# Kernel optimization log

Hardware: AMD Instinct MI355X
Metric: run time of the kernel (lower is better)

The kernel has to match this reference:

```python
import jax, jax.numpy as jnp
import numpy as np

NUM_EMBEDDINGS = 1024
EMBEDDING_DIM = 64
COMMITMENT_COST = 0.25


def setup_inputs() -> dict:
    key = jax.random.key(0)
    k1, k2 = jax.random.split(key)
    inputs = jax.random.normal(k1, (64, 2048, EMBEDDING_DIM), dtype=jnp.float32)
    # nn.Embedding weight init: uniform(-1/K, 1/K)
    lim = 1.0 / NUM_EMBEDDINGS
    weight = jax.random.uniform(k2, (NUM_EMBEDDINGS, EMBEDDING_DIM),
                                dtype=jnp.float32, minval=-lim, maxval=lim)
    return {"inputs": inputs, "weight": weight}


def reference(inputs, weight):
    # inputs: [B, T, D], weight: [K, D]
    flat = inputs.reshape(-1, EMBEDDING_DIM)              # [N, D]
    distances = (jnp.sum(flat * flat, axis=1, keepdims=True)
                 + jnp.sum(weight * weight, axis=1)
                 - 2.0 * flat @ weight.T)
    encoding_indices = jnp.argmin(distances, axis=1)[:, None]  # [N, 1]
    quantized = weight[encoding_indices[:, 0]].reshape(inputs.shape)
    # detached quantized vs inputs (commitment), quantized vs detached inputs (codebook)
    e_latent_loss = jnp.mean((jax.lax.stop_gradient(quantized) - inputs) ** 2)
    q_latent_loss = jnp.mean((quantized - jax.lax.stop_gradient(inputs)) ** 2)
    loss = q_latent_loss + COMMITMENT_COST * e_latent_loss
    # straight-through estimator
    quantized_st = inputs + jax.lax.stop_gradient(quantized - inputs)
    return (loss, quantized_st, encoding_indices)
```

## Files before the change

kernel.cpp:

```cpp
#include <hip/hip_runtime.h>

#define NROWS   131072
#define DIM     64
#define K       1024
#define QOFF    1
#define IDXOFF  8388609
#define NSCR    2048
#define NFIN    512

typedef float    f32x4 __attribute__((ext_vector_type(4)));
typedef _Float16 f16x8 __attribute__((ext_vector_type(8)));

__device__ __forceinline__ float np_norm64(const float* v) {
    #pragma clang fp contract(off)
    float r[8];
    #pragma unroll
    for (int k = 0; k < 8; ++k) r[k] = v[k] * v[k];
    #pragma unroll
    for (int i = 8; i < 64; i += 8)
        #pragma unroll
        for (int k = 0; k < 8; ++k) r[k] += v[i + k] * v[i + k];
    return ((r[0] + r[1]) + (r[2] + r[3])) + ((r[4] + r[5]) + (r[6] + r[7]));
}
__device__ __forceinline__ float exact_dot64(const float* xr, const float* __restrict__ e) {
    float a0 = 0.f, a1 = 0.f, a2 = 0.f, a3 = 0.f;
    #pragma unroll
    for (int i = 0; i < 64; i += 4) {
        a0 = fmaf(xr[i + 0], e[i + 0], a0);
        a1 = fmaf(xr[i + 1], e[i + 1], a1);
        a2 = fmaf(xr[i + 2], e[i + 2], a2);
        a3 = fmaf(xr[i + 3], e[i + 3], a3);
    }
    return (a0 + a1) + (a2 + a3);
}
__device__ __forceinline__ float exact_d(float cr, float sej, float dot) {
    #pragma clang fp contract(off)
    float t = cr + sej;
    return t - 2.0f * dot;
}

__global__ void vq_prep(const float* __restrict__ w, unsigned short* __restrict__ Gf,
                        float* __restrict__ wT, float* __restrict__ se,
                        float* __restrict__ se20) {
    int gid = blockIdx.x * 256 + threadIdx.x;
    int lane = gid & 63, c = (gid >> 6) & 1, ntile = gid >> 7;
    int code = ntile * 16 + (lane & 15);
    int k0 = c * 32 + (lane >> 4) * 8;
    const float* rowp = w + code * 64 + k0;
    f16x8 h8;
    #pragma unroll
    for (int j = 0; j < 8; ++j) h8[j] = (_Float16)(rowp[j] * 1024.0f);
    *(f16x8*)(Gf + gid * 8) = h8;
    #pragma unroll
    for (int t = 0; t < 8; ++t) {
        int flat = t * 8192 + gid;
        int i = flat >> 10, j = flat & 1023;
        wT[flat] = w[j * 64 + i];
    }
    if (gid < K) {
        #pragma clang fp contract(off)
        const float* e = w + gid * 64;
        float r[8];
        #pragma unroll
        for (int k2 = 0; k2 < 8; ++k2) r[k2] = e[k2] * e[k2];
        #pragma unroll
        for (int i = 8; i < 64; i += 8)
            #pragma unroll
            for (int k2 = 0; k2 < 8; ++k2) r[k2] += e[i + k2] * e[i + k2];
        float v = ((r[0] + r[1]) + (r[2] + r[3])) + ((r[4] + r[5]) + (r[6] + r[7]));
        se[gid] = v;
        se20[gid] = v * 1048576.0f;
    }
}

__global__ __launch_bounds__(256, 8) void vq_screen(
    const float* __restrict__ x, const float* __restrict__ w,
    const unsigned short* __restrict__ Gf, const float* __restrict__ se20,
    float* __restrict__ out, float* __restrict__ partial, int* __restrict__ gcnt,
    int* __restrict__ pairRows, int* __restrict__ pairJJ, int* __restrict__ fullRows) {
    __shared__ float sSe[1024];
    __shared__ float sPart[4];
    __shared__ int sCnt[2], sBase[2];
    __shared__ int sPairRow[64], sPairJJ[64], sFullRow[64];
    const int tid  = threadIdx.x;
    const int wave = tid >> 6, lane = tid & 63;
    const int quad = lane >> 4, m16 = lane & 15;
    const int wrow0 = blockIdx.x * 64 + wave * 16;

    if (tid < 2) sCnt[tid] = 0;
    #pragma unroll
    for (int t = 0; t < 4; ++t) sSe[t * 256 + tid] = se20[t * 256 + tid];

    f16x8 Ah[2];
    float Sloc = 0.f;
    #pragma unroll
    for (int c = 0; c < 2; ++c) {
        const float* p = x + (wrow0 + m16) * 64 + c * 32 + quad * 8;
        f32x4 u0 = *(const f32x4*)p;
        f32x4 u1 = *(const f32x4*)(p + 4);
        #pragma unroll
        for (int j = 0; j < 8; ++j) {
            float xv = (j < 4) ? u0[j] : u1[j - 4];
            Ah[c][j] = (_Float16)xv;
            Sloc += fabsf(xv);
        }
    }
    Sloc += __shfl_xor(Sloc, 16, 64);
    Sloc += __shfl_xor(Sloc, 32, 64);

    int m1[4], m2[4], m3[4];
    #pragma unroll
    for (int r = 0; r < 4; ++r) { m1[r] = 0x7fffffff; m2[r] = 0x7fffffff; m3[r] = 0x7fffffff; }

    __syncthreads();

    #pragma unroll 4
    for (int t = 0; t < 64; ++t) {
        f16x8 B0 = *(const f16x8*)(Gf + t * 1024 + lane * 8);
        f16x8 B1 = *(const f16x8*)(Gf + t * 1024 + 512 + lane * 8);
        float sen = sSe[t * 16 + m16];
        int jn = t * 16 + m16;
        f32x4 acc = {0.f, 0.f, 0.f, 0.f};
        acc = __builtin_amdgcn_mfma_f32_16x16x32_f16(Ah[0], B0, acc, 0, 0, 0);
        acc = __builtin_amdgcn_mfma_f32_16x16x32_f16(Ah[1], B1, acc, 0, 0, 0);
        #pragma unroll
        for (int r = 0; r < 4; ++r) {
            float kf = fmaf(acc[r], -2048.0f, sen);
            int q = (int)kf;
            int key = (int)((unsigned)q << 10) | jn;
            int a  = max(m2[r], key);
            int t2 = max(m1[r], key);
            m3[r] = min(m3[r], a);
            m2[r] = min(m2[r], t2);
            m1[r] = min(m1[r], key);
        }
    }

    #pragma unroll
    for (int mask = 1; mask <= 8; mask <<= 1) {
        #pragma unroll
        for (int r = 0; r < 4; ++r) {
            int b1 = __shfl_xor(m1[r], mask, 64);
            int b2 = __shfl_xor(m2[r], mask, 64);
            int b3 = __shfl_xor(m3[r], mask, 64);
            int lo1 = min(m1[r], b1), hi1 = max(m1[r], b1);
            int lo2 = min(m2[r], b2);
            m1[r] = lo1;
            m2[r] = min(hi1, lo2);
            m3[r] = min(max(hi1, lo2), min(m3[r], b3));
        }
    }

    int jd[4];
    #pragma unroll
    for (int r = 0; r < 4; ++r) {
        int k1 = m1[r], k2 = m2[r], k3 = m3[r];
        int g21 = (k2 >> 10) - (k1 >> 10);
        int g31 = (k3 >> 10) - (k1 >> 10);
        int j1 = k1 & 1023;
        float Srow = __shfl(Sloc, quad * 4 + r, 64);
        int mq = (int)(Srow * 2.002f) + 5;
        jd[r] = (g21 > mq) ? j1 : -1;
        if (m16 == 0) {
            int rowG = wrow0 + quad * 4 + r;
            if (g21 > mq) {
                out[IDXOFF + rowG] = (float)j1;
            } else if (g31 > mq) {
                int p = atomicAdd(&sCnt[0], 1);
                sPairRow[p] = rowG; sPairJJ[p] = j1 | ((k2 & 1023) << 10);
            } else {
                int p = atomicAdd(&sCnt[1], 1);
                sFullRow[p] = rowG;
            }
        }
    }

    float part = 0.f;
    #pragma unroll
    for (int i = 0; i < 16; ++i) {
        int jr = __shfl(jd[i & 3], (i >> 2) * 16, 64);
        if (jr >= 0) {
            #pragma clang fp contract(off)
            int rowG = wrow0 + i;
            float xv = x[rowG * 64 + lane];
            float wv = w[jr * 64 + lane];
            float diff = wv - xv;
            part += diff * diff;
            out[QOFF + rowG * 64 + lane] = xv + diff;
        }
    }
    for (int off = 32; off > 0; off >>= 1) part += __shfl_down(part, off, 64);
    if (lane == 0) sPart[wave] = part;
    __syncthreads();
    if (tid == 0) {
        partial[blockIdx.x] = (sPart[0] + sPart[1]) + (sPart[2] + sPart[3]);
        int np_ = sCnt[0], nf = sCnt[1];
        sBase[0] = np_ ? atomicAdd(&gcnt[0], np_) : 0;
        sBase[1] = nf  ? atomicAdd(&gcnt[1], nf)  : 0;
    }
    __syncthreads();
    if (tid < sCnt[0]) {
        int d = sBase[0] + tid;
        pairRows[d] = sPairRow[tid]; pairJJ[d] = sPairJJ[tid];
    }
    if (tid < sCnt[1]) fullRows[sBase[1] + tid] = sFullRow[tid];
}

__global__ __launch_bounds__(256) void vq_finish(
    const float* __restrict__ x, const float* __restrict__ w, const float* __restrict__ wT,
    const float* __restrict__ se, float* __restrict__ out, float* __restrict__ partial,
    const int* __restrict__ gcnt, const int* __restrict__ pairRows,
    const int* __restrict__ pairJJ, const int* __restrict__ fullRows) {
    __shared__ float sPart[4];
    const int tid = threadIdx.x;
    const int lane = tid & 63, wave = tid >> 6;
    const int nPair = gcnt[0], nFull = gcnt[1];
    const int gthread = blockIdx.x * 256 + tid, nThreads = gridDim.x * 256;
    const int gwave = blockIdx.x * 4 + wave,   nWaves = gridDim.x * 4;
    float part = 0.f;

    for (int i = gthread; i < nPair; i += nThreads) {
        int row = pairRows[i], jj = pairJJ[i];
        int ja = jj & 1023, jb = (jj >> 10) & 1023;
        if (ja > jb) { int t = ja; ja = jb; jb = t; }
        float xr[64];
        const f32x4* xp = (const f32x4*)(x + row * 64);
        #pragma unroll
        for (int t = 0; t < 16; ++t) {
            f32x4 v = xp[t];
            xr[4 * t] = v[0]; xr[4 * t + 1] = v[1]; xr[4 * t + 2] = v[2]; xr[4 * t + 3] = v[3];
        }
        float cr = np_norm64(xr);
        float da = exact_d(cr, se[ja], exact_dot64(xr, w + ja * 64));
        float db = exact_d(cr, se[jb], exact_dot64(xr, w + jb * 64));
        int win = (db < da) ? jb : ja;
        out[IDXOFF + row] = (float)win;
        const float* e = w + win * 64;
        {
            #pragma clang fp contract(off)
            #pragma unroll
            for (int i2 = 0; i2 < 64; ++i2) {
                float diff = e[i2] - xr[i2];
                part += diff * diff;
                out[QOFF + row * 64 + i2] = xr[i2] + diff;
            }
        }
    }

    const f32x4* wT4 = (const f32x4*)wT;
    for (int i = gwave; i < nFull; i += nWaves) {
        int row = fullRows[i];
        float xr[64];
        const f32x4* xp = (const f32x4*)(x + row * 64);
        #pragma unroll
        for (int t = 0; t < 16; ++t) {
            f32x4 v = xp[t];
            xr[4 * t] = v[0]; xr[4 * t + 1] = v[1]; xr[4 * t + 2] = v[2]; xr[4 * t + 3] = v[3];
        }
        float cr = np_norm64(xr);
        float bd = 3.402823466e38f; int bj = 0;
        #pragma unroll
        for (int g = 0; g < 4; ++g) {
            f32x4 a0 = {0.f,0.f,0.f,0.f}, a1 = a0, a2 = a0, a3 = a0;
            #pragma unroll 4
            for (int i2 = 0; i2 < 64; i2 += 4) {
                f32x4 w0 = wT4[(i2 + 0) * 256 + g * 64 + lane];
                f32x4 w1 = wT4[(i2 + 1) * 256 + g * 64 + lane];
                f32x4 w2 = wT4[(i2 + 2) * 256 + g * 64 + lane];
                f32x4 w3 = wT4[(i2 + 3) * 256 + g * 64 + lane];
                #pragma unroll
                for (int c = 0; c < 4; ++c) {
                    a0[c] = fmaf(xr[i2 + 0], w0[c], a0[c]);
                    a1[c] = fmaf(xr[i2 + 1], w1[c], a1[c]);
                    a2[c] = fmaf(xr[i2 + 2], w2[c], a2[c]);
                    a3[c] = fmaf(xr[i2 + 3], w3[c], a3[c]);
                }
            }
            #pragma unroll
            for (int c = 0; c < 4; ++c) {
                float dot = (a0[c] + a1[c]) + (a2[c] + a3[c]);
                int j = g * 256 + lane * 4 + c;
                float d = exact_d(cr, se[j], dot);
                if (d < bd) { bd = d; bj = j; }
            }
        }
        for (int mask = 1; mask < 64; mask <<= 1) {
            float od = __shfl_xor(bd, mask, 64);
            int   oj = __shfl_xor(bj, mask, 64);
            if (od < bd || (od == bd && oj < bj)) { bd = od; bj = oj; }
        }
        {
            #pragma clang fp contract(off)
            float xv = x[row * 64 + lane];
            float wv = w[bj * 64 + lane];
            float diff = wv - xv;
            part += diff * diff;
            out[QOFF + row * 64 + lane] = xv + diff;
        }
        if (lane == 0) out[IDXOFF + row] = (float)bj;
    }

    for (int off = 32; off > 0; off >>= 1) part += __shfl_down(part, off, 64);
    if (lane == 0) sPart[wave] = part;
    __syncthreads();
    if (tid == 0) partial[NSCR + blockIdx.x] = (sPart[0] + sPart[1]) + (sPart[2] + sPart[3]);
}

__global__ __launch_bounds__(256) void vq_loss(const float* __restrict__ partial,
                                               float* __restrict__ out) {
    __shared__ float red[4];
    const int tid = threadIdx.x, lane = tid & 63, wave = tid >> 6;
    float s = 0.f;
    #pragma unroll
    for (int t = 0; t < 10; ++t) s += partial[t * 256 + tid];
    for (int off = 32; off > 0; off >>= 1) s += __shfl_down(s, off, 64);
    if (lane == 0) red[wave] = s;
    __syncthreads();
    if (tid == 0) out[0] = ((red[0] + red[1]) + (red[2] + red[3])) * (1.25f / 8388608.0f);
}

extern "C" void kernel_launch(void* const* d_in, const int* in_sizes, int n_in,
                              void* d_out, int out_size, void* d_ws, size_t ws_size,
                              hipStream_t stream) {
    const float* x = (const float*)d_in[0];
    const float* w = (const float*)d_in[1];
    float* out = (float*)d_out;

    unsigned short* Gf = (unsigned short*)d_ws;
    float* se   = (float*)((char*)d_ws + 131072);
    float* se20 = (float*)((char*)d_ws + 135168);
    float* wT   = (float*)((char*)d_ws + 139264);
    int* gcnt   = (int*)((char*)d_ws + 401408);
    int* pairRows = (int*)((char*)d_ws + 401920);
    int* pairJJ   = pairRows + NROWS;
    int* fullRows = pairJJ + NROWS;
    float* partial = (float*)(fullRows + NROWS);

    (void)hipMemsetAsync(gcnt, 0, 2 * sizeof(int), stream);
    vq_prep<<<32, 256, 0, stream>>>(w, Gf, wT, se, se20);
    vq_screen<<<NSCR, 256, 0, stream>>>(x, w, Gf, se20, out, partial, gcnt,
                                        pairRows, pairJJ, fullRows);
    vq_finish<<<NFIN, 256, 0, stream>>>(x, w, wT, se, out, partial, gcnt,
                                        pairRows, pairJJ, fullRows);
    vq_loss<<<1, 256, 0, stream>>>(partial, out);
}
```

Baseline: 185.9 us.

## Screen two row tiles per wave to reuse codebook fragments; fold counter reset into prep

Each screening wave now handles 32 rows as two 16-row MFMA tiles that share the same codebook B-fragment loads, so the grid is halved and Gf traffic per row is halved. Launch bounds are relaxed to 4 blocks per SM to fit the doubled register state. The loss reduction loop is resized to the new partial count. The separate memset of the global counters is removed and the reset is done inside the prep kernel, saving one enqueue. The cost is higher register pressure and lower occupancy.

```diff
diff --git a/kernel.cpp b/kernel.cpp
--- a/kernel.cpp
+++ b/kernel.cpp
@@ -5,7 +5,7 @@
 #define K       1024
 #define QOFF    1
 #define IDXOFF  8388609
-#define NSCR    2048
+#define NSCR    1024
 #define NFIN    512
 
 typedef float    f32x4 __attribute__((ext_vector_type(4)));
@@ -41,8 +41,9 @@
 
 __global__ void vq_prep(const float* __restrict__ w, unsigned short* __restrict__ Gf,
                         float* __restrict__ wT, float* __restrict__ se,
-                        float* __restrict__ se20) {
+                        float* __restrict__ se20, int* __restrict__ gcnt) {
     int gid = blockIdx.x * 256 + threadIdx.x;
+    if (gid < 2) gcnt[gid] = 0;
     int lane = gid & 63, c = (gid >> 6) & 1, ntile = gid >> 7;
     int code = ntile * 16 + (lane & 15);
     int k0 = c * 32 + (lane >> 4) * 8;
@@ -73,7 +74,7 @@
     }
 }
 
-__global__ __launch_bounds__(256, 8) void vq_screen(
+__global__ __launch_bounds__(256, 4) void vq_screen(
     const float* __restrict__ x, const float* __restrict__ w,
     const unsigned short* __restrict__ Gf, const float* __restrict__ se20,
     float* __restrict__ out, float* __restrict__ partial, int* __restrict__ gcnt,
@@ -81,104 +82,120 @@
     __shared__ float sSe[1024];
     __shared__ float sPart[4];
     __shared__ int sCnt[2], sBase[2];
-    __shared__ int sPairRow[64], sPairJJ[64], sFullRow[64];
+    __shared__ int sPairRow[128], sPairJJ[128], sFullRow[128];
     const int tid  = threadIdx.x;
     const int wave = tid >> 6, lane = tid & 63;
     const int quad = lane >> 4, m16 = lane & 15;
-    const int wrow0 = blockIdx.x * 64 + wave * 16;
+    const int wrow0 = blockIdx.x * 128 + wave * 32;
 
     if (tid < 2) sCnt[tid] = 0;
     #pragma unroll
     for (int t = 0; t < 4; ++t) sSe[t * 256 + tid] = se20[t * 256 + tid];
 
-    f16x8 Ah[2];
-    float Sloc = 0.f;
-    #pragma unroll
-    for (int c = 0; c < 2; ++c) {
-        const float* p = x + (wrow0 + m16) * 64 + c * 32 + quad * 8;
-        f32x4 u0 = *(const f32x4*)p;
-        f32x4 u1 = *(const f32x4*)(p + 4);
-        #pragma unroll
-        for (int j = 0; j < 8; ++j) {
-            float xv = (j < 4) ? u0[j] : u1[j - 4];
-            Ah[c][j] = (_Float16)xv;
-            Sloc += fabsf(xv);
-        }
-    }
-    Sloc += __shfl_xor(Sloc, 16, 64);
-    Sloc += __shfl_xor(Sloc, 32, 64);
-
-    int m1[4], m2[4], m3[4];
-    #pragma unroll
-    for (int r = 0; r < 4; ++r) { m1[r] = 0x7fffffff; m2[r] = 0x7fffffff; m3[r] = 0x7fffffff; }
-
-    __syncthreads();
-
-    #pragma unroll 4
+    f16x8 Ah[2][2];
+    float Sloc[2] = {0.f, 0.f};
+    #pragma unroll
+    for (int mt = 0; mt < 2; ++mt)
+        #pragma unroll
+        for (int c = 0; c < 2; ++c) {
+            const float* p = x + (wrow0 + mt * 16 + m16) * 64 + c * 32 + quad * 8;
+            f32x4 u0 = *(const f32x4*)p;
+            f32x4 u1 = *(const f32x4*)(p + 4);
+            #pragma unroll
+            for (int j = 0; j < 8; ++j) {
+                float xv = (j < 4) ? u0[j] : u1[j - 4];
+                Ah[mt][c][j] = (_Float16)xv;
+                Sloc[mt] += fabsf(xv);
+            }
+        }
+    #pragma unroll
+    for (int mt = 0; mt < 2; ++mt) {
+        Sloc[mt] += __shfl_xor(Sloc[mt], 16, 64);
+        Sloc[mt] += __shfl_xor(Sloc[mt], 32, 64);
+    }
+
+    int m1[2][4], m2[2][4], m3[2][4];
+    #pragma unroll
+    for (int mt = 0; mt < 2; ++mt)
+        #pragma unroll
+        for (int r = 0; r < 4; ++r) {
+            m1[mt][r] = 0x7fffffff; m2[mt][r] = 0x7fffffff; m3[mt][r] = 0x7fffffff;
+        }
+
+    __syncthreads();
+
+    #pragma unroll 8
     for (int t = 0; t < 64; ++t) {
         f16x8 B0 = *(const f16x8*)(Gf + t * 1024 + lane * 8);
         f16x8 B1 = *(const f16x8*)(Gf + t * 1024 + 512 + lane * 8);
         float sen = sSe[t * 16 + m16];
         int jn = t * 16 + m16;
-        f32x4 acc = {0.f, 0.f, 0.f, 0.f};
-        acc = __builtin_amdgcn_mfma_f32_16x16x32_f16(Ah[0], B0, acc, 0, 0, 0);
-        acc = __builtin_amdgcn_mfma_f32_16x16x32_f16(Ah[1], B1, acc, 0, 0, 0);
+        #pragma unroll
+        for (int mt = 0; mt < 2; ++mt) {
+            f32x4 acc = {0.f, 0.f, 0.f, 0.f};
+            acc = __builtin_amdgcn_mfma_f32_16x16x32_f16(Ah[mt][0], B0, acc, 0, 0, 0);
+            acc = __builtin_amdgcn_mfma_f32_16x16x32_f16(Ah[mt][1], B1, acc, 0, 0, 0);
+            #pragma unroll
+            for (int r = 0; r < 4; ++r) {
+                float kf = fmaf(acc[r], -2048.0f, sen);
+                int q = (int)kf;
+                int key = (int)((unsigned)q << 10) | jn;
+                int a  = max(m2[mt][r], key);
+                int t2 = max(m1[mt][r], key);
+                m3[mt][r] = min(m3[mt][r], a);
+                m2[mt][r] = min(m2[mt][r], t2);
+                m1[mt][r] = min(m1[mt][r], key);
+            }
+        }
+    }
+
+    #pragma unroll
+    for (int mask = 1; mask <= 8; mask <<= 1) {
+        #pragma unroll
+        for (int mt = 0; mt < 2; ++mt)
+            #pragma unroll
+            for (int r = 0; r < 4; ++r) {
+                int b1 = __shfl_xor(m1[mt][r], mask, 64);
+                int b2 = __shfl_xor(m2[mt][r], mask, 64);
+                int b3 = __shfl_xor(m3[mt][r], mask, 64);
+                int lo1 = min(m1[mt][r], b1), hi1 = max(m1[mt][r], b1);
+                int lo2 = min(m2[mt][r], b2);
+                m1[mt][r] = lo1;
+                m2[mt][r] = min(hi1, lo2);
+                m3[mt][r] = min(max(hi1, lo2), min(m3[mt][r], b3));
+            }
+    }
+
+    int jd[2][4];
+    #pragma unroll
+    for (int mt = 0; mt < 2; ++mt)
         #pragma unroll
         for (int r = 0; r < 4; ++r) {
-            float kf = fmaf(acc[r], -2048.0f, sen);
-            int q = (int)kf;
-            int key = (int)((unsigned)q << 10) | jn;
-            int a  = max(m2[r], key);
-            int t2 = max(m1[r], key);
-            m3[r] = min(m3[r], a);
-            m2[r] = min(m2[r], t2);
-            m1[r] = min(m1[r], key);
-        }
-    }
-
-    #pragma unroll
-    for (int mask = 1; mask <= 8; mask <<= 1) {
-        #pragma unroll
-        for (int r = 0; r < 4; ++r) {
-            int b1 = __shfl_xor(m1[r], mask, 64);
-            int b2 = __shfl_xor(m2[r], mask, 64);
-            int b3 = __shfl_xor(m3[r], mask, 64);
-            int lo1 = min(m1[r], b1), hi1 = max(m1[r], b1);
-            int lo2 = min(m2[r], b2);
-            m1[r] = lo1;
-            m2[r] = min(hi1, lo2);
-            m3[r] = min(max(hi1, lo2), min(m3[r], b3));
-        }
-    }
-
-    int jd[4];
-    #pragma unroll
-    for (int r = 0; r < 4; ++r) {
-        int k1 = m1[r], k2 = m2[r], k3 = m3[r];
-        int g21 = (k2 >> 10) - (k1 >> 10);
-        int g31 = (k3 >> 10) - (k1 >> 10);
-        int j1 = k1 & 1023;
-        float Srow = __shfl(Sloc, quad * 4 + r, 64);
-        int mq = (int)(Srow * 2.002f) + 5;
-        jd[r] = (g21 > mq) ? j1 : -1;
-        if (m16 == 0) {
-            int rowG = wrow0 + quad * 4 + r;
-            if (g21 > mq) {
-                out[IDXOFF + rowG] = (float)j1;
-            } else if (g31 > mq) {
-                int p = atomicAdd(&sCnt[0], 1);
-                sPairRow[p] = rowG; sPairJJ[p] = j1 | ((k2 & 1023) << 10);
-            } else {
-                int p = atomicAdd(&sCnt[1], 1);
-                sFullRow[p] = rowG;
-            }
-        }
-    }
+            int k1 = m1[mt][r], k2 = m2[mt][r], k3 = m3[mt][r];
+            int g21 = (k2 >> 10) - (k1 >> 10);
+            int g31 = (k3 >> 10) - (k1 >> 10);
+            int j1 = k1 & 1023;
+            float Srow = __shfl(Sloc[mt], quad * 4 + r, 64);
+            int mq = (int)(Srow * 2.002f) + 5;
+            jd[mt][r] = (g21 > mq) ? j1 : -1;
+            if (m16 == 0) {
+                int rowG = wrow0 + mt * 16 + quad * 4 + r;
+                if (g21 > mq) {
+                    out[IDXOFF + rowG] = (float)j1;
+                } else if (g31 > mq) {
+                    int p = atomicAdd(&sCnt[0], 1);
+                    sPairRow[p] = rowG; sPairJJ[p] = j1 | ((k2 & 1023) << 10);
+                } else {
+                    int p = atomicAdd(&sCnt[1], 1);
+                    sFullRow[p] = rowG;
+                }
+            }
+        }
 
     float part = 0.f;
     #pragma unroll
-    for (int i = 0; i < 16; ++i) {
-        int jr = __shfl(jd[i & 3], (i >> 2) * 16, 64);
+    for (int i = 0; i < 32; ++i) {
+        int jr = __shfl(jd[i >> 4][i & 3], ((i & 15) >> 2) * 16, 64);
         if (jr >= 0) {
             #pragma clang fp contract(off)
             int rowG = wrow0 + i;
@@ -312,7 +329,7 @@
     const int tid = threadIdx.x, lane = tid & 63, wave = tid >> 6;
     float s = 0.f;
     #pragma unroll
-    for (int t = 0; t < 10; ++t) s += partial[t * 256 + tid];
+    for (int t = 0; t < 6; ++t) s += partial[t * 256 + tid];
     for (int off = 32; off > 0; off >>= 1) s += __shfl_down(s, off, 64);
     if (lane == 0) red[wave] = s;
     __syncthreads();
@@ -336,8 +353,7 @@
     int* fullRows = pairJJ + NROWS;
     float* partial = (float*)(fullRows + NROWS);
 
-    (void)hipMemsetAsync(gcnt, 0, 2 * sizeof(int), stream);
-    vq_prep<<<32, 256, 0, stream>>>(w, Gf, wT, se, se20);
+    vq_prep<<<32, 256, 0, stream>>>(w, Gf, wT, se, se20, gcnt);
     vq_screen<<<NSCR, 256, 0, stream>>>(x, w, Gf, se20, out, partial, gcnt,
                                         pairRows, pairJJ, fullRows);
     vq_finish<<<NFIN, 256, 0, stream>>>(x, w, wT, se, out, partial, gcnt,
```

New measurement: 184.7 us. About the same (-0.6%).
